# Performance work log

Measured on AMD Instinct MI355X. Metric: run time of the kernel, lower is better.

The kernel has to match this reference:

```python
import jax, jax.numpy as jnp
import numpy as np


def setup_inputs() -> dict:
    key = jax.random.key(0)
    k1, k2, k3 = jax.random.split(key, 3)
    inp = jax.random.normal(k1, (32, 128, 56, 56), dtype=jnp.float32)
    # kaiming-style scale for a 3x3 conv kernel
    fan_in = 128 * 3 * 3
    kernel = jax.random.normal(k2, (256, 128, 3, 3), dtype=jnp.float32) * np.float32(np.sqrt(2.0 / fan_in))
    bias = jax.random.normal(k3, (256,), dtype=jnp.float32)
    return {"inp": inp, "kernel": kernel, "bias": bias}


def reference(inp, kernel, bias):
    # 3x3 conv, stride 1, padding 1 (SAME), NCHW / OIHW layout, plus bias.
    out = jax.lax.conv_general_dilated(
        inp, kernel,
        window_strides=(1, 1),
        padding=((1, 1), (1, 1)),
        dimension_numbers=("NCHW", "OIHW", "NCHW"),
    )
    return out + bias[None, :, None, None]
```

## Files before the change

kernel.cpp:

```cpp
#include <hip/hip_runtime.h>
#include <hip/hip_bf16.h>


#define C_IN   128
#define K_OUT  256
#define HW     56
#define IMG    3136
#define NBATCH 32
#define PW     58
#define KTOT   1152
#define IN_WS_USHORT ((size_t)4*NBATCH*PW*256*8)
#define WT_WS_USHORT ((size_t)12*3072*8)

typedef __bf16 bf16x8 __attribute__((ext_vector_type(8)));
typedef float  f32x4  __attribute__((ext_vector_type(4)));
typedef unsigned short ushort8 __attribute__((ext_vector_type(8)));

__device__ inline unsigned short f2bf(float f) {
    unsigned int u = __builtin_bit_cast(unsigned int, f);
    u += ((u >> 16) & 1u) + 0x7FFFu;
    return (unsigned short)(u >> 16);
}

__device__ __forceinline__ void gl2lds16(const unsigned short* g, unsigned short* l) {
    __builtin_amdgcn_global_load_lds(
        (const __attribute__((address_space(1))) unsigned int*)g,
        (__attribute__((address_space(3))) unsigned int*)l, 16, 0, 0);
}

__global__ void prep_input(const float* __restrict__ inp,
                           unsigned short* __restrict__ dst) {
    __shared__ unsigned short tile[C_IN * 57];
    int n = blockIdx.x / PW, py = blockIdx.x % PW;
    ushort8* d8 = (ushort8*)dst;
    const bool border = (py == 0 || py == PW - 1);
    if (!border) {
        const float* src = inp + (size_t)n * C_IN * IMG + (py - 1) * HW;
        for (int i = threadIdx.x; i < C_IN * HW; i += 256) {
            int c = i / HW, x = i - c * HW;
            tile[c * 57 + x] = f2bf(src[c * IMG + x]);
        }
        __syncthreads();
    }
    for (int i = threadIdx.x; i < 1024; i += 256) {
        int cq = i >> 8, rem = i & 255;
        int X = ((rem >> 6) & 3) * 16 + (rem & 15);
        int cc = (rem >> 4) & 3;
        ushort8 v = (ushort8)0;
        if (!border && X >= 1 && X <= HW) {
#pragma unroll
            for (int e = 0; e < 8; ++e)
                v[e] = tile[(cq * 32 + cc * 8 + e) * 57 + (X - 1)];
        }
        d8[((size_t)(cq * NBATCH + n) * PW + py) * 256 + rem] = v;
    }
}

__global__ void prep_weights(const float* __restrict__ w,
                             unsigned short* __restrict__ dst) {
    int idx = blockIdx.x * 256 + threadIdx.x;
    int chunk = idx >> 3, e = idx & 7;
    int p = chunk / 3072, rem = chunk - p * 3072;
    int s = rem >> 10, rem2 = rem & 1023;
    int koq = rem2 >> 6, cc = (rem2 >> 4) & 3, kor = rem2 & 15;
    int ko = koq * 16 + kor;
    int cq = p / 3, r = p - 3 * cq;
    int c = cq * 32 + cc * 8 + e;
    dst[idx] = f2bf(w[(ko * C_IN + c) * 9 + r * 3 + s]);
}

__global__ __launch_bounds__(512, 2) void conv_mfma(
        const unsigned short* __restrict__ In,
        const unsigned short* __restrict__ Wt,
        const float* __restrict__ bias,
        float* __restrict__ out) {
    __shared__ unsigned short smem[73728];

    const int tid = threadIdx.x;
    const int lane = tid & 63, wv = tid >> 6;
    const int l15 = lane & 15, lk = lane >> 4;
    const int blk = blockIdx.x;
    const int n = blk / 14, rb = (blk % 14) * 4;

    const int wko = (wv & 3) * 64;
    const int wpx = (wv >> 2) * 112;
    const int albase = (wv & 3) * 4096 + lk * 256 + l15 * 16;

    int addrB[3][7];
#pragma unroll
    for (int nf = 0; nf < 7; ++nf) {
        int p = wpx + nf * 16 + l15;
        int yl = p / 56, x = p - yl * 56;
#pragma unroll
        for (int s = 0; s < 3; ++s) {
            int X = x + s;
            addrB[s][nf] = yl * 4096 + (X >> 4) * 1024 + lk * 256 + (X & 15) * 16;
        }
    }

    f32x4 acc[4][7];
#pragma unroll
    for (int m = 0; m < 4; ++m)
#pragma unroll
        for (int nf = 0; nf < 7; ++nf) acc[m][nf] = (f32x4)0.0f;

#define STAGE_W(PHN) do {                                                   \
    _Pragma("unroll")                                                       \
    for (int li = 0; li < 6; ++li) {                                        \
        int chunk = li * 512 + tid;                                         \
        gl2lds16(Wt + (PHN) * 24576 + chunk * 8,                            \
                 &smem[((PHN) & 1) * 24576 + chunk * 8]);                   \
    } } while (0)

#define STAGE_I(CQN, R_) do {                                               \
    int chunk = (R_) * 512 + tid;                                           \
    gl2lds16(In + ((size_t)((CQN) * NBATCH + n) * PW + rb) * 2048 + chunk * 8, \
             &smem[49152 + ((CQN) & 1) * 12288 + chunk * 8]);               \
} while (0)

    STAGE_W(0);
    STAGE_I(0, 0); STAGE_I(0, 1); STAGE_I(0, 2);

#define PHASE(PH) do {                                                      \
    constexpr int cq_ = (PH) / 3, r_ = (PH) % 3;                            \
    if ((PH) < 11) { STAGE_W((PH) + 1); }                                   \
    if (cq_ < 3)   { STAGE_I(cq_ + 1, r_); }                                \
    asm volatile("s_waitcnt vmcnt(%0)"                                      \
                 :: "i"((PH) < 9 ? 7 : ((PH) < 11 ? 6 : 0)) : "memory");    \
    __builtin_amdgcn_s_barrier();                                           \
    { const char* wb = (const char*)smem + ((PH) & 1) * 49152;              \
      const char* ib = (const char*)smem + 98304 + (cq_ & 1) * 24576;       \
      __builtin_amdgcn_s_setprio(1);                                        \
      _Pragma("unroll")                                                     \
      for (int s = 0; s < 3; ++s) {                                         \
          bf16x8 a[4], b[7];                                                \
          _Pragma("unroll")                                                 \
          for (int m = 0; m < 4; ++m)                                       \
              a[m] = *(const bf16x8*)(wb + albase + s * 16384 + m * 1024);  \
          _Pragma("unroll")                                                 \
          for (int nf = 0; nf < 7; ++nf)                                    \
              b[nf] = *(const bf16x8*)(ib + addrB[s][nf] + r_ * 4096);      \
          _Pragma("unroll")                                                 \
          for (int m = 0; m < 4; ++m)                                       \
              _Pragma("unroll")                                             \
              for (int nf = 0; nf < 7; ++nf)                                \
                  acc[m][nf] = __builtin_amdgcn_mfma_f32_16x16x32_bf16(     \
                      a[m], b[nf], acc[m][nf], 0, 0, 0);                    \
      }                                                                     \
      __builtin_amdgcn_s_setprio(0);                                        \
    }                                                                       \
    __builtin_amdgcn_s_barrier();                                           \
} while (0)

    PHASE(0);  PHASE(1);  PHASE(2);  PHASE(3);
    PHASE(4);  PHASE(5);  PHASE(6);  PHASE(7);
    PHASE(8);  PHASE(9);  PHASE(10); PHASE(11);

#undef PHASE
#undef STAGE_I
#undef STAGE_W

    const int sp0 = rb * 56 + wpx;
#pragma unroll
    for (int m = 0; m < 4; ++m) {
        int kb = wko + m * 16 + lk * 4;
        f32x4 bs = *(const f32x4*)(bias + kb);
#pragma unroll
        for (int nf = 0; nf < 7; ++nf) {
            float* ob = out + ((size_t)(n * K_OUT + kb) * IMG) + sp0 + nf * 16 + l15;
#pragma unroll
            for (int j = 0; j < 4; ++j)
                ob[(size_t)j * IMG] = acc[m][nf][j] + bs[j];
        }
    }
}

__global__ void conv_naive(const float* __restrict__ inp,
                           const float* __restrict__ ker,
                           const float* __restrict__ bias,
                           float* __restrict__ out, int total) {
    int o = blockIdx.x * blockDim.x + threadIdx.x;
    if (o >= total) return;
    int x = o % HW, y = (o / HW) % HW, ko = (o / IMG) % K_OUT, n = o / (IMG * K_OUT);
    float acc = bias[ko];
    for (int c = 0; c < C_IN; ++c)
        for (int r = 0; r < 3; ++r) {
            int iy = y + r - 1; if ((unsigned)iy >= HW) continue;
            for (int s = 0; s < 3; ++s) {
                int ix = x + s - 1; if ((unsigned)ix >= HW) continue;
                acc += inp[((n * C_IN + c) * HW + iy) * HW + ix]
                     * ker[((ko * C_IN + c) * 3 + r) * 3 + s];
            }
        }
    out[o] = acc;
}

extern "C" void kernel_launch(void* const* d_in, const int* in_sizes, int n_in,
                              void* d_out, int out_size, void* d_ws, size_t ws_size,
                              hipStream_t stream) {
    const float* inp  = (const float*)d_in[0];
    const float* ker  = (const float*)d_in[1];
    const float* bias = (const float*)d_in[2];
    float* out = (float*)d_out;

    const size_t need = (IN_WS_USHORT + WT_WS_USHORT) * 2;
    if (ws_size < need) {
        int total = NBATCH * K_OUT * IMG;
        conv_naive<<<(total + 255) / 256, 256, 0, stream>>>(inp, ker, bias, out, total);
        return;
    }

    unsigned short* inb = (unsigned short*)d_ws;
    unsigned short* wtb = inb + IN_WS_USHORT;

    prep_input<<<NBATCH * PW, 256, 0, stream>>>(inp, inb);
    prep_weights<<<(K_OUT * KTOT) / 256, 256, 0, stream>>>(ker, wtb);

    conv_mfma<<<448, 512, 0, stream>>>(inb, wtb, bias, out);
}
```

Baseline: 83.53 us.

## Split output channels across two blocks and stage input as ring of rows

Each block now covers 128 output channels instead of 256, giving 896 blocks of 256 threads with half the shared memory, which lets more blocks share a CU. Input staging becomes an 8-slot ring of individual padded rows, so each row is loaded once per channel quarter rather than as overlapping three-row windows, and the weight layout is reordered per channel half. The cost is that every input tile is now read by two blocks, and row addresses are computed per phase.

```diff
diff --git a/kernel.cpp b/kernel.cpp
--- a/kernel.cpp
+++ b/kernel.cpp
@@ -10,7 +10,7 @@
 #define PW     58
 #define KTOT   1152
 #define IN_WS_USHORT ((size_t)4*NBATCH*PW*256*8)
-#define WT_WS_USHORT ((size_t)12*3072*8)
+#define WT_WS_USHORT ((size_t)12*2*1536*8)
 
 typedef __bf16 bf16x8 __attribute__((ext_vector_type(8)));
 typedef float  f32x4  __attribute__((ext_vector_type(4)));
@@ -61,40 +61,43 @@
     int idx = blockIdx.x * 256 + threadIdx.x;
     int chunk = idx >> 3, e = idx & 7;
     int p = chunk / 3072, rem = chunk - p * 3072;
-    int s = rem >> 10, rem2 = rem & 1023;
-    int koq = rem2 >> 6, cc = (rem2 >> 4) & 3, kor = rem2 & 15;
-    int ko = koq * 16 + kor;
+    int koh = rem / 1536, rem2 = rem - koh * 1536;
+    int s = rem2 / 512, rem3 = rem2 - s * 512;
+    int koq = rem3 >> 6, cc = (rem3 >> 4) & 3, kor = rem3 & 15;
+    int ko = koh * 128 + koq * 16 + kor;
     int cq = p / 3, r = p - 3 * cq;
     int c = cq * 32 + cc * 8 + e;
     dst[idx] = f2bf(w[(ko * C_IN + c) * 9 + r * 3 + s]);
 }
 
-__global__ __launch_bounds__(512, 2) void conv_mfma(
+__global__ __launch_bounds__(256, 2) void conv_mfma(
         const unsigned short* __restrict__ In,
         const unsigned short* __restrict__ Wt,
         const float* __restrict__ bias,
         float* __restrict__ out) {
-    __shared__ unsigned short smem[73728];
+    __shared__ unsigned short smem[40960];
 
     const int tid = threadIdx.x;
     const int lane = tid & 63, wv = tid >> 6;
     const int l15 = lane & 15, lk = lane >> 4;
-    const int blk = blockIdx.x;
-    const int n = blk / 14, rb = (blk % 14) * 4;
-
-    const int wko = (wv & 3) * 64;
-    const int wpx = (wv >> 2) * 112;
-    const int albase = (wv & 3) * 4096 + lk * 256 + l15 * 16;
-
-    int addrB[3][7];
+    const int koh = blockIdx.x;
+    const int by = blockIdx.y;
+    const int n = by / 14, rb = (by % 14) * 4;
+
+    const int wkol = (wv & 1) * 64;
+    const int wpx  = (wv >> 1) * 112;
+    const int albase = (wv & 1) * 4096 + lk * 256 + l15 * 16;
+
+    int yl[7], xp[3][7];
 #pragma unroll
     for (int nf = 0; nf < 7; ++nf) {
         int p = wpx + nf * 16 + l15;
-        int yl = p / 56, x = p - yl * 56;
+        yl[nf] = p / 56;
+        int x = p - yl[nf] * 56;
 #pragma unroll
         for (int s = 0; s < 3; ++s) {
             int X = x + s;
-            addrB[s][nf] = yl * 4096 + (X >> 4) * 1024 + lk * 256 + (X & 15) * 16;
+            xp[s][nf] = ((X >> 4) << 10) + lk * 256 + ((X & 15) << 4);
         }
     }
 
@@ -107,39 +110,52 @@
 #define STAGE_W(PHN) do {                                                   \
     _Pragma("unroll")                                                       \
     for (int li = 0; li < 6; ++li) {                                        \
-        int chunk = li * 512 + tid;                                         \
-        gl2lds16(Wt + (PHN) * 24576 + chunk * 8,                            \
-                 &smem[((PHN) & 1) * 24576 + chunk * 8]);                   \
+        int chunk = li * 256 + tid;                                         \
+        gl2lds16(Wt + ((size_t)((PHN) * 2 + koh)) * 12288 + chunk * 8,      \
+                 &smem[((PHN) & 1) * 12288 + chunk * 8]);                   \
     } } while (0)
 
-#define STAGE_I(CQN, R_) do {                                               \
-    int chunk = (R_) * 512 + tid;                                           \
-    gl2lds16(In + ((size_t)((CQN) * NBATCH + n) * PW + rb) * 2048 + chunk * 8, \
-             &smem[49152 + ((CQN) & 1) * 12288 + chunk * 8]);               \
+#define STAGE_ROW(C_, T_) do {                                              \
+    gl2lds16(In + ((size_t)(((C_) * NBATCH + n) * PW + rb + (T_))) * 2048 + tid * 8, \
+             &smem[24576 + ((6 * (C_) + (T_)) & 7) * 2048 + tid * 8]);      \
 } while (0)
 
     STAGE_W(0);
-    STAGE_I(0, 0); STAGE_I(0, 1); STAGE_I(0, 2);
+    STAGE_ROW(0, 0); STAGE_ROW(0, 1); STAGE_ROW(0, 2); STAGE_ROW(0, 3);
 
 #define PHASE(PH) do {                                                      \
     constexpr int cq_ = (PH) / 3, r_ = (PH) % 3;                            \
-    if ((PH) < 11) { STAGE_W((PH) + 1); }                                   \
-    if (cq_ < 3)   { STAGE_I(cq_ + 1, r_); }                                \
-    asm volatile("s_waitcnt vmcnt(%0)"                                      \
-                 :: "i"((PH) < 9 ? 7 : ((PH) < 11 ? 6 : 0)) : "memory");    \
+    if ((PH) < 11) STAGE_W((PH) + 1);                                       \
+    if constexpr (r_ == 0) {                                                \
+        if constexpr (cq_ < 3) { STAGE_ROW(cq_ + 1, 0); STAGE_ROW(cq_ + 1, 1); } \
+        STAGE_ROW(cq_, 4);                                                  \
+    } else if constexpr (r_ == 1) {                                         \
+        if constexpr (cq_ < 3) STAGE_ROW(cq_ + 1, 2);                       \
+        STAGE_ROW(cq_, 5);                                                  \
+    } else {                                                                \
+        if constexpr (cq_ < 3) STAGE_ROW(cq_ + 1, 3);                       \
+    }                                                                       \
+    { constexpr int nIss = ((PH) < 11 ? 6 : 0) +                            \
+          (r_ == 0 ? (cq_ < 3 ? 3 : 1) : r_ == 1 ? (cq_ < 3 ? 2 : 1)        \
+                                       : (cq_ < 3 ? 1 : 0));                \
+      asm volatile("s_waitcnt vmcnt(%0)" :: "i"(nIss) : "memory"); }        \
     __builtin_amdgcn_s_barrier();                                           \
-    { const char* wb = (const char*)smem + ((PH) & 1) * 49152;              \
-      const char* ib = (const char*)smem + 98304 + (cq_ & 1) * 24576;       \
+    { const char* wb = (const char*)smem + ((PH) & 1) * 24576;              \
+      const char* ib = (const char*)smem + 49152;                           \
+      int roff[7];                                                          \
+      _Pragma("unroll")                                                     \
+      for (int nf = 0; nf < 7; ++nf)                                        \
+          roff[nf] = ((6 * cq_ + r_ + yl[nf]) & 7) << 12;                   \
       __builtin_amdgcn_s_setprio(1);                                        \
       _Pragma("unroll")                                                     \
       for (int s = 0; s < 3; ++s) {                                         \
           bf16x8 a[4], b[7];                                                \
           _Pragma("unroll")                                                 \
           for (int m = 0; m < 4; ++m)                                       \
-              a[m] = *(const bf16x8*)(wb + albase + s * 16384 + m * 1024);  \
+              a[m] = *(const bf16x8*)(wb + albase + s * 8192 + m * 1024);   \
           _Pragma("unroll")                                                 \
           for (int nf = 0; nf < 7; ++nf)                                    \
-              b[nf] = *(const bf16x8*)(ib + addrB[s][nf] + r_ * 4096);      \
+              b[nf] = *(const bf16x8*)(ib + roff[nf] + xp[s][nf]);          \
           _Pragma("unroll")                                                 \
           for (int m = 0; m < 4; ++m)                                       \
               _Pragma("unroll")                                             \
@@ -157,13 +173,13 @@
     PHASE(8);  PHASE(9);  PHASE(10); PHASE(11);
 
 #undef PHASE
-#undef STAGE_I
+#undef STAGE_ROW
 #undef STAGE_W
 
     const int sp0 = rb * 56 + wpx;
 #pragma unroll
     for (int m = 0; m < 4; ++m) {
-        int kb = wko + m * 16 + lk * 4;
+        int kb = koh * 128 + wkol + m * 16 + lk * 4;
         f32x4 bs = *(const f32x4*)(bias + kb);
 #pragma unroll
         for (int nf = 0; nf < 7; ++nf) {
@@ -214,7 +230,7 @@
     unsigned short* wtb = inb + IN_WS_USHORT;
 
     prep_input<<<NBATCH * PW, 256, 0, stream>>>(inp, inb);
-    prep_weights<<<(K_OUT * KTOT) / 256, 256, 0, stream>>>(ker, wtb);
-
-    conv_mfma<<<448, 512, 0, stream>>>(inb, wtb, bias, out);
-}
+    prep_weights<<<(int)(WT_WS_USHORT / 256), 256, 0, stream>>>(ker, wtb);
+
+    conv_mfma<<<dim3(2, 448), 256, 0, stream>>>(inb, wtb, bias, out);
+}
```

New measurement: 81.15 us. 1.03x faster.
